# Kernel optimization log

Hardware: AMD Instinct MI355X
Metric: run time of the kernel (lower is better)

## Reference

```python
import jax, jax.numpy as jnp
import numpy as np

GRID = 32  # hard-coded voxel resolution in the original module


def setup_inputs() -> dict:
    key = jax.random.key(0)
    k1, k2 = jax.random.split(key)
    points = jax.random.normal(k1, (4, 100000, 3), dtype=jnp.float32)
    features = jax.random.normal(k2, (4, 100000, 64), dtype=jnp.float32)
    return {"points": points, "features": features}


def reference(points, features):
    # points: [B, N, 3], features: [B, N, F]
    B, N, _ = points.shape
    Fdim = features.shape[-1]
    # Global (over whole tensor) min/max normalization, exactly as original
    pmin = points.min()
    pmax = points.max()
    normed = (points - pmin) / (pmax - pmin + 1e-6)  # in [0, 1)
    # torch: (normed // (1/32)).long() == floor(normed * 32)
    vox = jnp.floor(normed * GRID).astype(jnp.int32)  # [B, N, 3], values in [0, 31]
    gidx = vox[..., 0] * (GRID * GRID) + vox[..., 1] * GRID + vox[..., 2]  # [B, N]
    # Scatter-max into a zero-initialized grid (zeros init == implicit max with 0,
    # matching the original torch.zeros output_grid).
    grid = jnp.zeros((B, GRID ** 3, Fdim), dtype=features.dtype)
    batch_ids = jnp.arange(B, dtype=jnp.int32)[:, None]  # [B, 1] broadcast over N
    grid = grid.at[batch_ids, gidx].max(features)
    return grid.reshape(B, GRID, GRID, GRID, Fdim)
```

## Files before the change

kernel.cpp:

```cpp
#include <hip/hip_runtime.h>

#define GRID3 32768
#define FDIM 64

__device__ __forceinline__ unsigned int enc_f32(float f) {
    unsigned int u = __float_as_uint(f);
    return (u & 0x80000000u) ? ~u : (u | 0x80000000u);
}
__device__ __forceinline__ float dec_f32(unsigned int u) {
    u = (u & 0x80000000u) ? (u ^ 0x80000000u) : ~u;
    return __uint_as_float(u);
}

__global__ void init_ws_kernel(unsigned int* ws) {
    ws[0] = 0xFFFFFFFFu;
    ws[1] = 0u;
}

__global__ void minmax_kernel(const float* __restrict__ pts, int n,
                              unsigned int* __restrict__ ws) {
    float lmin = INFINITY, lmax = -INFINITY;
    for (int i = blockIdx.x * blockDim.x + threadIdx.x; i < n;
         i += gridDim.x * blockDim.x) {
        float v = pts[i];
        lmin = fminf(lmin, v);
        lmax = fmaxf(lmax, v);
    }
    __shared__ float smin[256], smax[256];
    smin[threadIdx.x] = lmin;
    smax[threadIdx.x] = lmax;
    __syncthreads();
    for (int s = 128; s > 0; s >>= 1) {
        if (threadIdx.x < (unsigned)s) {
            smin[threadIdx.x] = fminf(smin[threadIdx.x], smin[threadIdx.x + s]);
            smax[threadIdx.x] = fmaxf(smax[threadIdx.x], smax[threadIdx.x + s]);
        }
        __syncthreads();
    }
    if (threadIdx.x == 0) {
        atomicMin(&ws[0], enc_f32(smin[0]));
        atomicMax(&ws[1], enc_f32(smax[0]));
    }
}

__global__ void scatter_kernel(const float* __restrict__ pts,
                               const float* __restrict__ feat,
                               const unsigned int* __restrict__ ws,
                               unsigned int* __restrict__ out,
                               int ntot, int N) {
    int lane = threadIdx.x & 63;
    int p = blockIdx.x * 4 + (threadIdx.x >> 6);
    if (p >= ntot) return;

    float pmin = dec_f32(ws[0]);
    float pmax = dec_f32(ws[1]);
    float denom = pmax - pmin + 1e-6f;

    float x = pts[p * 3 + 0];
    float y = pts[p * 3 + 1];
    float z = pts[p * 3 + 2];

    int vx = (int)floorf(((x - pmin) / denom) * 32.0f);
    int vy = (int)floorf(((y - pmin) / denom) * 32.0f);
    int vz = (int)floorf(((z - pmin) / denom) * 32.0f);
    vx = min(max(vx, 0), 31);
    vy = min(max(vy, 0), 31);
    vz = min(max(vz, 0), 31);
    int gidx = vx * 1024 + vy * 32 + vz;

    int b = p / N;
    float f = feat[(size_t)p * FDIM + lane];

    if (f > 0.0f) {
        unsigned int* addr = out + ((size_t)b * GRID3 + gidx) * FDIM + lane;
        atomicMax(addr, __float_as_uint(f));
    }
}

extern "C" void kernel_launch(void* const* d_in, const int* in_sizes, int n_in,
                              void* d_out, int out_size, void* d_ws, size_t ws_size,
                              hipStream_t stream) {
    const float* pts = (const float*)d_in[0];
    const float* feat = (const float*)d_in[1];
    unsigned int* ws = (unsigned int*)d_ws;

    int npts3 = in_sizes[0];
    int ntot = npts3 / 3;
    int B = out_size / (GRID3 * FDIM);
    int N = ntot / B;

    hipLaunchKernelGGL(init_ws_kernel, dim3(1), dim3(1), 0, stream, ws);
    hipLaunchKernelGGL(minmax_kernel, dim3(512), dim3(256), 0, stream,
                       pts, npts3, ws);
    hipMemsetAsync(d_out, 0, (size_t)out_size * sizeof(float), stream);
    int blocks = (ntot + 3) / 4;
    hipLaunchKernelGGL(scatter_kernel, dim3(blocks), dim3(256), 0, stream,
                       pts, feat, ws, (unsigned int*)d_out, ntot, N);
}
```

Before: 250.2 us.

## Replace atomic scatter-max with counting-sort binning and per-voxel gather-max

Points are counted per (batch, voxel) bin, a three-kernel prefix scan builds bin offsets, and a point order array is filled by bin. A gather kernel then reduces the features of each bin directly into the output. This removes the full-output memset and per-element atomicMax traffic, and every output element is written exactly once. In exchange it launches several more kernels, needs extra workspace (falling back to the old path if that is too small), and does random feature reads in the gather. The min/max pass also reads the points as float4.

Measured after the change: 380.8 us. +52.2%, slower.

```diff
diff --git a/kernel.cpp b/kernel.cpp
--- a/kernel.cpp
+++ b/kernel.cpp
@@ -1,7 +1,8 @@
 #include <hip/hip_runtime.h>
 
-#define GRID3 32768
-#define FDIM 64
+#define SPATIAL 32768
+#define NBINS   131072
+#define FDIM    64
 
 __device__ __forceinline__ unsigned int enc_f32(float f) {
     unsigned int u = __float_as_uint(f);
@@ -12,19 +13,20 @@
     return __uint_as_float(u);
 }
 
-__global__ void init_ws_kernel(unsigned int* ws) {
-    ws[0] = 0xFFFFFFFFu;
-    ws[1] = 0u;
-}
-
-__global__ void minmax_kernel(const float* __restrict__ pts, int n,
-                              unsigned int* __restrict__ ws) {
+
+__global__ void init_ws_kernel(unsigned int* mm) {
+    mm[0] = 0xFFFFFFFFu;
+    mm[1] = 0u;
+}
+
+__global__ void minmax_kernel(const float4* __restrict__ pts4, int n4,
+                              unsigned int* __restrict__ mm) {
     float lmin = INFINITY, lmax = -INFINITY;
-    for (int i = blockIdx.x * blockDim.x + threadIdx.x; i < n;
+    for (int i = blockIdx.x * blockDim.x + threadIdx.x; i < n4;
          i += gridDim.x * blockDim.x) {
-        float v = pts[i];
-        lmin = fminf(lmin, v);
-        lmax = fmaxf(lmax, v);
+        float4 v = pts4[i];
+        lmin = fminf(fminf(lmin, v.x), fminf(v.y, v.z)); lmin = fminf(lmin, v.w);
+        lmax = fmaxf(fmaxf(lmax, v.x), fmaxf(v.y, v.z)); lmax = fmaxf(lmax, v.w);
     }
     __shared__ float smin[256], smax[256];
     smin[threadIdx.x] = lmin;
@@ -38,28 +40,138 @@
         __syncthreads();
     }
     if (threadIdx.x == 0) {
-        atomicMin(&ws[0], enc_f32(smin[0]));
-        atomicMax(&ws[1], enc_f32(smax[0]));
-    }
+        atomicMin(&mm[0], enc_f32(smin[0]));
+        atomicMax(&mm[1], enc_f32(smax[0]));
+    }
+}
+
+__global__ void bincount_kernel(const float* __restrict__ pts,
+                                const unsigned int* __restrict__ mm,
+                                unsigned int* __restrict__ counts,
+                                unsigned int* __restrict__ binof,
+                                int ntot, int N) {
+    int p = blockIdx.x * blockDim.x + threadIdx.x;
+    if (p >= ntot) return;
+    float pmin = dec_f32(mm[0]);
+    float pmax = dec_f32(mm[1]);
+    float denom = pmax - pmin + 1e-6f;
+
+    float x = pts[p * 3 + 0];
+    float y = pts[p * 3 + 1];
+    float z = pts[p * 3 + 2];
+    int vx = (int)floorf(((x - pmin) / denom) * 32.0f);
+    int vy = (int)floorf(((y - pmin) / denom) * 32.0f);
+    int vz = (int)floorf(((z - pmin) / denom) * 32.0f);
+    vx = min(max(vx, 0), 31);
+    vy = min(max(vy, 0), 31);
+    vz = min(max(vz, 0), 31);
+    int b = p / N;
+    unsigned int bin = (unsigned)b * SPATIAL + vx * 1024 + vy * 32 + vz;
+    binof[p] = bin;
+    atomicAdd(&counts[bin], 1u);
+}
+
+__global__ void scan_blocksums_kernel(const unsigned int* __restrict__ counts,
+                                      unsigned int* __restrict__ bsum) {
+    __shared__ unsigned int s[256];
+    int i = blockIdx.x * 256 + threadIdx.x;
+    s[threadIdx.x] = counts[i];
+    __syncthreads();
+    for (int st = 128; st > 0; st >>= 1) {
+        if (threadIdx.x < (unsigned)st) s[threadIdx.x] += s[threadIdx.x + st];
+        __syncthreads();
+    }
+    if (threadIdx.x == 0) bsum[blockIdx.x] = s[0];
+}
+
+__global__ void scan_top_kernel(unsigned int* __restrict__ bsum,
+                                unsigned int* __restrict__ boff) {
+    __shared__ unsigned int s[512];
+    unsigned int v = bsum[threadIdx.x];
+    s[threadIdx.x] = v;
+    __syncthreads();
+    for (int st = 1; st < 512; st <<= 1) {
+        unsigned int add = (threadIdx.x >= (unsigned)st) ? s[threadIdx.x - st] : 0u;
+        __syncthreads();
+        s[threadIdx.x] += add;
+        __syncthreads();
+    }
+    boff[threadIdx.x] = s[threadIdx.x] - v;
+}
+
+__global__ void scan_write_kernel(const unsigned int* __restrict__ counts,
+                                  const unsigned int* __restrict__ boff,
+                                  unsigned int* __restrict__ offsets,
+                                  unsigned int* __restrict__ cursor) {
+    __shared__ unsigned int s[256];
+    int i = blockIdx.x * 256 + threadIdx.x;
+    unsigned int v = counts[i];
+    s[threadIdx.x] = v;
+    __syncthreads();
+    for (int st = 1; st < 256; st <<= 1) {
+        unsigned int add = (threadIdx.x >= (unsigned)st) ? s[threadIdx.x - st] : 0u;
+        __syncthreads();
+        s[threadIdx.x] += add;
+        __syncthreads();
+    }
+    unsigned int off = boff[blockIdx.x] + s[threadIdx.x] - v;
+    offsets[i] = off;
+    cursor[i] = off;
+}
+
+__global__ void build_order_kernel(const unsigned int* __restrict__ binof,
+                                   unsigned int* __restrict__ cursor,
+                                   unsigned int* __restrict__ order,
+                                   int ntot) {
+    int p = blockIdx.x * blockDim.x + threadIdx.x;
+    if (p >= ntot) return;
+    unsigned int bin = binof[p];
+    unsigned int pos = atomicAdd(&cursor[bin], 1u);
+    order[pos] = (unsigned)p;
+}
+
+__global__ void gather_kernel(const float* __restrict__ feat,
+                              const unsigned int* __restrict__ counts,
+                              const unsigned int* __restrict__ offsets,
+                              const unsigned int* __restrict__ order,
+                              float* __restrict__ out) {
+    int gtid = blockIdx.x * blockDim.x + threadIdx.x;
+    int bin = gtid >> 6;
+    int lane = threadIdx.x & 63;
+    if (bin >= NBINS) return;
+
+    unsigned int cnt = counts[bin];
+    unsigned int off = offsets[bin];
+
+    float m0 = 0.0f, m1 = 0.0f;
+    unsigned int i = 0;
+    for (; i + 1 < cnt; i += 2) {
+        unsigned int p0 = order[off + i];
+        unsigned int p1 = order[off + i + 1];
+        float f0 = feat[(size_t)p0 * FDIM + lane];
+        float f1 = feat[(size_t)p1 * FDIM + lane];
+        m0 = fmaxf(m0, f0);
+        m1 = fmaxf(m1, f1);
+    }
+    if (i < cnt) {
+        unsigned int p0 = order[off + i];
+        m0 = fmaxf(m0, feat[(size_t)p0 * FDIM + lane]);
+    }
+    out[(size_t)bin * FDIM + lane] = fmaxf(m0, m1);
 }
 
 __global__ void scatter_kernel(const float* __restrict__ pts,
                                const float* __restrict__ feat,
-                               const unsigned int* __restrict__ ws,
+                               const unsigned int* __restrict__ mm,
                                unsigned int* __restrict__ out,
                                int ntot, int N) {
     int lane = threadIdx.x & 63;
     int p = blockIdx.x * 4 + (threadIdx.x >> 6);
     if (p >= ntot) return;
-
-    float pmin = dec_f32(ws[0]);
-    float pmax = dec_f32(ws[1]);
+    float pmin = dec_f32(mm[0]);
+    float pmax = dec_f32(mm[1]);
     float denom = pmax - pmin + 1e-6f;
-
-    float x = pts[p * 3 + 0];
-    float y = pts[p * 3 + 1];
-    float z = pts[p * 3 + 2];
-
+    float x = pts[p * 3 + 0], y = pts[p * 3 + 1], z = pts[p * 3 + 2];
     int vx = (int)floorf(((x - pmin) / denom) * 32.0f);
     int vy = (int)floorf(((y - pmin) / denom) * 32.0f);
     int vz = (int)floorf(((z - pmin) / denom) * 32.0f);
@@ -67,13 +179,11 @@
     vy = min(max(vy, 0), 31);
     vz = min(max(vz, 0), 31);
     int gidx = vx * 1024 + vy * 32 + vz;
-
     int b = p / N;
     float f = feat[(size_t)p * FDIM + lane];
-
     if (f > 0.0f) {
-        unsigned int* addr = out + ((size_t)b * GRID3 + gidx) * FDIM + lane;
-        atomicMax(addr, __float_as_uint(f));
+        atomicMax(out + ((size_t)b * SPATIAL + gidx) * FDIM + lane,
+                  __float_as_uint(f));
     }
 }
 
@@ -82,18 +192,49 @@
                               hipStream_t stream) {
     const float* pts = (const float*)d_in[0];
     const float* feat = (const float*)d_in[1];
-    unsigned int* ws = (unsigned int*)d_ws;
 
     int npts3 = in_sizes[0];
     int ntot = npts3 / 3;
-    int B = out_size / (GRID3 * FDIM);
+    int B = out_size / (SPATIAL * FDIM);
     int N = ntot / B;
 
-    hipLaunchKernelGGL(init_ws_kernel, dim3(1), dim3(1), 0, stream, ws);
+    unsigned int* ws = (unsigned int*)d_ws;
+    unsigned int* counts  = ws;
+    unsigned int* cursor  = ws + NBINS;
+    unsigned int* offsets = ws + 2 * NBINS;
+    unsigned int* binof   = ws + 3 * NBINS;
+    unsigned int* order   = binof + ntot;
+    unsigned int* mm      = order + ntot;
+    unsigned int* bsum    = mm + 2;
+    unsigned int* boff    = bsum + 512;
+
+    size_t need = ((size_t)3 * NBINS + 2 * (size_t)ntot + 2 + 1024) * 4;
+    if (ws_size < need) {
+        unsigned int* mm2 = ws;
+        hipLaunchKernelGGL(init_ws_kernel, dim3(1), dim3(1), 0, stream, mm2);
+        hipLaunchKernelGGL(minmax_kernel, dim3(512), dim3(256), 0, stream,
+                           (const float4*)pts, npts3 / 4, mm2);
+        hipMemsetAsync(d_out, 0, (size_t)out_size * sizeof(float), stream);
+        hipLaunchKernelGGL(scatter_kernel, dim3((ntot + 3) / 4), dim3(256), 0,
+                           stream, pts, feat, mm2, (unsigned int*)d_out, ntot, N);
+        return;
+    }
+
+    hipMemsetAsync(counts, 0, (size_t)NBINS * 4, stream);
+    hipLaunchKernelGGL(init_ws_kernel, dim3(1), dim3(1), 0, stream, mm);
     hipLaunchKernelGGL(minmax_kernel, dim3(512), dim3(256), 0, stream,
-                       pts, npts3, ws);
-    hipMemsetAsync(d_out, 0, (size_t)out_size * sizeof(float), stream);
-    int blocks = (ntot + 3) / 4;
-    hipLaunchKernelGGL(scatter_kernel, dim3(blocks), dim3(256), 0, stream,
-                       pts, feat, ws, (unsigned int*)d_out, ntot, N);
-}
+                       (const float4*)pts, npts3 / 4, mm);
+    int pblocks = (ntot + 255) / 256;
+    hipLaunchKernelGGL(bincount_kernel, dim3(pblocks), dim3(256), 0, stream,
+                       pts, mm, counts, binof, ntot, N);
+    hipLaunchKernelGGL(scan_blocksums_kernel, dim3(NBINS / 256), dim3(256), 0,
+                       stream, counts, bsum);
+    hipLaunchKernelGGL(scan_top_kernel, dim3(1), dim3(512), 0, stream,
+                       bsum, boff);
+    hipLaunchKernelGGL(scan_write_kernel, dim3(NBINS / 256), dim3(256), 0,
+                       stream, counts, boff, offsets, cursor);
+    hipLaunchKernelGGL(build_order_kernel, dim3(pblocks), dim3(256), 0, stream,
+                       binof, cursor, order, ntot);
+    hipLaunchKernelGGL(gather_kernel, dim3(NBINS * 64 / 256), dim3(256), 0,
+                       stream, feat, counts, offsets, order, (float*)d_out);
+}
```

## Bin points by voxel via counting sort, then reduce per-bin before atomics

Applied to the files above, without the earlier changes.

Replaces the direct per-point atomicMax scatter with a counting sort. Points are binned by (batch, voxel), bins get offsets, an ordering array is built, and a gather pass runs per wave: it reads features in sorted order, takes a running max across consecutive points in the same bin, and issues one atomicMax per bin segment. The phases are fused into one cooperative kernel with grid syncs, and the min/max pass is vectorised with float4 and wave shuffles. This is meant to cut atomic contention on the output grid. The cost is extra passes over the points, a workspace-dependent path, and feature reads that become scattered by point index.

Measured after the change: 748.7 us. 2.99x slower.

```diff
diff --git a/kernel.cpp b/kernel.cpp
--- a/kernel.cpp
+++ b/kernel.cpp
@@ -1,80 +1,219 @@
 #include <hip/hip_runtime.h>
-
-#define GRID3 32768
-#define FDIM 64
-
-__device__ __forceinline__ unsigned int enc_f32(float f) {
-    unsigned int u = __float_as_uint(f);
+#include <hip/hip_cooperative_groups.h>
+
+namespace cg = cooperative_groups;
+
+#define SPATIAL 32768
+#define NBINS   131072
+#define FDIM    64
+#define BLOCKS  1024
+#define TPB     256
+#define NTHREADS (BLOCKS * TPB)
+
+
+__device__ __forceinline__ unsigned enc_f32(float f) {
+    unsigned u = __float_as_uint(f);
     return (u & 0x80000000u) ? ~u : (u | 0x80000000u);
 }
-__device__ __forceinline__ float dec_f32(unsigned int u) {
+__device__ __forceinline__ float dec_f32(unsigned u) {
     u = (u & 0x80000000u) ? (u ^ 0x80000000u) : ~u;
     return __uint_as_float(u);
 }
 
-__global__ void init_ws_kernel(unsigned int* ws) {
-    ws[0] = 0xFFFFFFFFu;
-    ws[1] = 0u;
-}
-
-__global__ void minmax_kernel(const float* __restrict__ pts, int n,
-                              unsigned int* __restrict__ ws) {
-    float lmin = INFINITY, lmax = -INFINITY;
-    for (int i = blockIdx.x * blockDim.x + threadIdx.x; i < n;
-         i += gridDim.x * blockDim.x) {
-        float v = pts[i];
-        lmin = fminf(lmin, v);
-        lmax = fmaxf(lmax, v);
-    }
-    __shared__ float smin[256], smax[256];
-    smin[threadIdx.x] = lmin;
-    smax[threadIdx.x] = lmax;
-    __syncthreads();
-    for (int s = 128; s > 0; s >>= 1) {
-        if (threadIdx.x < (unsigned)s) {
-            smin[threadIdx.x] = fminf(smin[threadIdx.x], smin[threadIdx.x + s]);
-            smax[threadIdx.x] = fmaxf(smax[threadIdx.x], smax[threadIdx.x + s]);
-        }
-        __syncthreads();
-    }
-    if (threadIdx.x == 0) {
-        atomicMin(&ws[0], enc_f32(smin[0]));
-        atomicMax(&ws[1], enc_f32(smax[0]));
-    }
-}
-
-__global__ void scatter_kernel(const float* __restrict__ pts,
-                               const float* __restrict__ feat,
-                               const unsigned int* __restrict__ ws,
-                               unsigned int* __restrict__ out,
-                               int ntot, int N) {
-    int lane = threadIdx.x & 63;
-    int p = blockIdx.x * 4 + (threadIdx.x >> 6);
-    if (p >= ntot) return;
-
-    float pmin = dec_f32(ws[0]);
-    float pmax = dec_f32(ws[1]);
-    float denom = pmax - pmin + 1e-6f;
-
+__device__ __forceinline__ unsigned compute_bin(const float* __restrict__ pts,
+                                                int p, int N,
+                                                float pmin, float denom) {
     float x = pts[p * 3 + 0];
     float y = pts[p * 3 + 1];
     float z = pts[p * 3 + 2];
-
     int vx = (int)floorf(((x - pmin) / denom) * 32.0f);
     int vy = (int)floorf(((y - pmin) / denom) * 32.0f);
     int vz = (int)floorf(((z - pmin) / denom) * 32.0f);
     vx = min(max(vx, 0), 31);
     vy = min(max(vy, 0), 31);
     vz = min(max(vz, 0), 31);
-    int gidx = vx * 1024 + vy * 32 + vz;
-
     int b = p / N;
+    return (unsigned)b * SPATIAL + (unsigned)(vx * 1024 + vy * 32 + vz);
+}
+
+
+__device__ void ph_minmax(const float* __restrict__ pts, int n,
+                          unsigned* __restrict__ mm, int tid, int nthreads) {
+    float lmin = INFINITY, lmax = -INFINITY;
+    int n4 = n >> 2;
+    const float4* p4 = (const float4*)pts;
+    for (int i = tid; i < n4; i += nthreads) {
+        float4 v = p4[i];
+        lmin = fminf(fminf(lmin, v.x), fminf(v.y, v.z)); lmin = fminf(lmin, v.w);
+        lmax = fmaxf(fmaxf(lmax, v.x), fmaxf(v.y, v.z)); lmax = fmaxf(lmax, v.w);
+    }
+    for (int i = (n4 << 2) + tid; i < n; i += nthreads) {
+        float v = pts[i];
+        lmin = fminf(lmin, v); lmax = fmaxf(lmax, v);
+    }
+#pragma unroll
+    for (int d = 1; d < 64; d <<= 1) {
+        lmin = fminf(lmin, __shfl_xor(lmin, d, 64));
+        lmax = fmaxf(lmax, __shfl_xor(lmax, d, 64));
+    }
+    if ((threadIdx.x & 63) == 0) {
+        atomicMin(&mm[0], enc_f32(lmin));
+        atomicMin(&mm[1], ~enc_f32(lmax));
+    }
+}
+
+__device__ void ph_bincount(const float* __restrict__ pts,
+                            const unsigned* __restrict__ mm,
+                            unsigned* __restrict__ counts,
+                            int ntot, int N, int tid, int nthreads) {
+    float pmin = dec_f32(mm[0]);
+    float denom = dec_f32(~mm[1]) - pmin + 1e-6f;
+    for (int p = tid; p < ntot; p += nthreads) {
+        unsigned bin = compute_bin(pts, p, N, pmin, denom);
+        atomicAdd(&counts[bin], 1u);
+    }
+}
+
+__device__ void ph_offsets(unsigned* __restrict__ counts,
+                           unsigned* __restrict__ tail, int tid, int nthreads) {
+    int lane = threadIdx.x & 63;
+    for (int i = tid; i < NBINS; i += nthreads) {
+        unsigned cnt = counts[i];
+        unsigned cs = cnt;
+#pragma unroll
+        for (int d = 1; d < 64; d <<= 1) {
+            unsigned v = __shfl_up(cs, (unsigned)d, 64);
+            if (lane >= d) cs += v;
+        }
+        unsigned ctot = __shfl(cs, 63, 64);
+        unsigned base = 0;
+        if (lane == 63 && ctot) base = atomicAdd(tail, ctot);
+        base = __shfl(base, 63, 64);
+        if (cnt) counts[i] = base + cs - cnt;
+    }
+}
+
+__device__ void ph_build(const float* __restrict__ pts,
+                         const unsigned* __restrict__ mm,
+                         unsigned* __restrict__ cursor,
+                         uint2* __restrict__ ord2,
+                         int ntot, int N, int tid, int nthreads) {
+    float pmin = dec_f32(mm[0]);
+    float denom = dec_f32(~mm[1]) - pmin + 1e-6f;
+    for (int p = tid; p < ntot; p += nthreads) {
+        unsigned bin = compute_bin(pts, p, N, pmin, denom);
+        unsigned pos = atomicAdd(&cursor[bin], 1u);
+        ord2[pos] = make_uint2((unsigned)p, bin);
+    }
+}
+
+__device__ void ph_gather(const float* __restrict__ feat,
+                          const uint2* __restrict__ ord2,
+                          int ntot, unsigned* __restrict__ out,
+                          int tid, int nthreads) {
+    int lane = threadIdx.x & 63;
+    unsigned wave = (unsigned)tid >> 6;
+    unsigned nwaves = (unsigned)nthreads >> 6;
+    unsigned nchunks = ((unsigned)ntot + 63u) >> 6;
+
+    for (unsigned c = wave; c < nchunks; c += nwaves) {
+        unsigned base = c << 6;
+        unsigned nb = min(64u, (unsigned)ntot - base);
+        uint2 e = (lane < (int)nb) ? ord2[base + lane]
+                                   : make_uint2(0u, 0xFFFFFFFFu);
+        unsigned pv = e.x;
+        unsigned bv = e.y;
+
+        float m = 0.0f;
+        for (unsigned j0 = 0; j0 < nb; j0 += 16) {
+            unsigned kn = min(16u, nb - j0);
+            float f[16];
+#pragma unroll
+            for (unsigned k = 0; k < 16; ++k) {
+                if (k < kn) {
+                    unsigned p = __shfl(pv, (int)(j0 + k), 64);
+                    f[k] = feat[(size_t)p * FDIM + lane];
+                }
+            }
+#pragma unroll
+            for (unsigned k = 0; k < 16; ++k) {
+                if (k < kn) {
+                    unsigned idx = j0 + k;
+                    unsigned b  = __shfl(bv, (int)idx, 64);
+                    unsigned bn = (idx + 1 < nb) ? __shfl(bv, (int)(idx + 1), 64)
+                                                 : 0xFFFFFFFFu;
+                    m = fmaxf(m, f[k]);
+                    if (b != bn) {
+                        if (m > 0.0f)
+                            atomicMax(&out[(size_t)b * FDIM + lane],
+                                      __float_as_uint(m));
+                        m = 0.0f;
+                    }
+                }
+            }
+        }
+    }
+}
+
+__global__ void __launch_bounds__(TPB, 4)
+fused_kernel(const float* __restrict__ pts, const float* __restrict__ feat,
+             unsigned* __restrict__ ws, unsigned* __restrict__ out,
+             int ntot, int npts3, int N) {
+    cg::grid_group grid = cg::this_grid();
+    int tid = blockIdx.x * blockDim.x + threadIdx.x;
+    unsigned* counts = ws;
+    unsigned* tail   = ws + NBINS;
+    unsigned* mm     = ws + NBINS + 1;
+    uint2*    ord2   = (uint2*)(ws + NBINS + 4);
+
+    ph_minmax(pts, npts3, mm, tid, NTHREADS);
+    grid.sync();
+    ph_bincount(pts, mm, counts, ntot, N, tid, NTHREADS);
+    grid.sync();
+    ph_offsets(counts, tail, tid, NTHREADS);
+    grid.sync();
+    ph_build(pts, mm, counts, ord2, ntot, N, tid, NTHREADS);
+    grid.sync();
+    ph_gather(feat, ord2, ntot, out, tid, NTHREADS);
+}
+
+__global__ void k_minmax(const float* pts, int n, unsigned* mm) {
+    ph_minmax(pts, n, mm, blockIdx.x * blockDim.x + threadIdx.x,
+              gridDim.x * blockDim.x);
+}
+__global__ void k_bincount(const float* pts, const unsigned* mm,
+                           unsigned* counts, int ntot, int N) {
+    ph_bincount(pts, mm, counts, ntot, N,
+                blockIdx.x * blockDim.x + threadIdx.x, gridDim.x * blockDim.x);
+}
+__global__ void k_offsets(unsigned* counts, unsigned* tail) {
+    ph_offsets(counts, tail, blockIdx.x * blockDim.x + threadIdx.x,
+               gridDim.x * blockDim.x);
+}
+__global__ void k_build(const float* pts, const unsigned* mm, unsigned* cursor,
+                        uint2* ord2, int ntot, int N) {
+    ph_build(pts, mm, cursor, ord2, ntot, N,
+             blockIdx.x * blockDim.x + threadIdx.x, gridDim.x * blockDim.x);
+}
+__global__ void k_gather(const float* feat, const uint2* ord2, int ntot,
+                         unsigned* out) {
+    ph_gather(feat, ord2, ntot, out,
+              blockIdx.x * blockDim.x + threadIdx.x, gridDim.x * blockDim.x);
+}
+
+__global__ void scatter_kernel(const float* __restrict__ pts,
+                               const float* __restrict__ feat,
+                               const unsigned* __restrict__ mm,
+                               unsigned* __restrict__ out, int ntot, int N) {
+    int lane = threadIdx.x & 63;
+    int p = blockIdx.x * 4 + (threadIdx.x >> 6);
+    if (p >= ntot) return;
+    float pmin = dec_f32(mm[0]);
+    float denom = dec_f32(~mm[1]) - pmin + 1e-6f;
+    unsigned bin = compute_bin(pts, p, N, pmin, denom);
     float f = feat[(size_t)p * FDIM + lane];
-
-    if (f > 0.0f) {
-        unsigned int* addr = out + ((size_t)b * GRID3 + gidx) * FDIM + lane;
-        atomicMax(addr, __float_as_uint(f));
-    }
+    if (f > 0.0f)
+        atomicMax(&out[(size_t)bin * FDIM + lane], __float_as_uint(f));
 }
 
 extern "C" void kernel_launch(void* const* d_in, const int* in_sizes, int n_in,
@@ -82,18 +221,51 @@
                               hipStream_t stream) {
     const float* pts = (const float*)d_in[0];
     const float* feat = (const float*)d_in[1];
-    unsigned int* ws = (unsigned int*)d_ws;
 
     int npts3 = in_sizes[0];
     int ntot = npts3 / 3;
-    int B = out_size / (GRID3 * FDIM);
+    int B = out_size / (SPATIAL * FDIM);
     int N = ntot / B;
 
-    hipLaunchKernelGGL(init_ws_kernel, dim3(1), dim3(1), 0, stream, ws);
-    hipLaunchKernelGGL(minmax_kernel, dim3(512), dim3(256), 0, stream,
-                       pts, npts3, ws);
+    unsigned* ws = (unsigned*)d_ws;
+    unsigned* counts = ws;
+    unsigned* tail   = ws + NBINS;
+    unsigned* mm     = ws + NBINS + 1;
+    uint2*    ord2   = (uint2*)(ws + NBINS + 4);
+    unsigned* outp   = (unsigned*)d_out;
+
+    hipMemsetAsync(counts, 0, ((size_t)NBINS + 1) * 4, stream);
+    hipMemsetAsync(mm, 0xFF, 8, stream);
     hipMemsetAsync(d_out, 0, (size_t)out_size * sizeof(float), stream);
-    int blocks = (ntot + 3) / 4;
-    hipLaunchKernelGGL(scatter_kernel, dim3(blocks), dim3(256), 0, stream,
-                       pts, feat, ws, (unsigned int*)d_out, ntot, N);
-}
+
+    size_t need = ((size_t)NBINS + 4 + 2 * (size_t)ntot) * 4;
+    if (ws_size < need) {
+        hipLaunchKernelGGL(k_minmax, dim3(512), dim3(256), 0, stream,
+                           pts, npts3, mm);
+        hipLaunchKernelGGL(scatter_kernel, dim3((ntot + 3) / 4), dim3(256), 0,
+                           stream, pts, feat, mm, outp, ntot, N);
+        return;
+    }
+
+    int dev = 0, coop = 0;
+    (void)hipGetDevice(&dev);
+    (void)hipDeviceGetAttribute(&coop, hipDeviceAttributeCooperativeLaunch, dev);
+
+    if (coop) {
+        void* args[] = {(void*)&pts, (void*)&feat, (void*)&ws, (void*)&outp,
+                        (void*)&ntot, (void*)&npts3, (void*)&N};
+        hipLaunchCooperativeKernel((void*)fused_kernel, dim3(BLOCKS), dim3(TPB),
+                                   args, 0, stream);
+    } else {
+        hipLaunchKernelGGL(k_minmax, dim3(BLOCKS), dim3(TPB), 0, stream,
+                           pts, npts3, mm);
+        hipLaunchKernelGGL(k_bincount, dim3(BLOCKS), dim3(TPB), 0, stream,
+                           pts, mm, counts, ntot, N);
+        hipLaunchKernelGGL(k_offsets, dim3(BLOCKS), dim3(TPB), 0, stream,
+                           counts, tail);
+        hipLaunchKernelGGL(k_build, dim3(BLOCKS), dim3(TPB), 0, stream,
+                           pts, mm, counts, ord2, ntot, N);
+        hipLaunchKernelGGL(k_gather, dim3(BLOCKS), dim3(TPB), 0, stream,
+                           feat, ord2, ntot, outp);
+    }
+}
```
